# Optimization experiments

Hardware: AMD Instinct MI355X
Metric: run time of the kernel (lower is better)

Reference implementation:

```python
import jax, jax.numpy as jnp
import numpy as np

NUM_L, NUM_W = 10, 10  # num_points_lw


def _local_coords():
    # torch.cartesian_prod(linspace_l, linspace_w) -> (P, 2), l varies slowest
    l = jnp.linspace(-0.5, 0.5, NUM_L)
    w = jnp.linspace(-0.5, 0.5, NUM_W)
    L, W = jnp.meshgrid(l, w, indexing='ij')
    return jnp.stack([L.reshape(-1), W.reshape(-1)], axis=-1)  # (P, 2)


def setup_inputs() -> dict:
    key = jax.random.key(0)
    k1, k2, k3 = jax.random.split(key, 3)
    B, N, T, H, W = 32, 8, 52, 224, 224
    # trajectory states (x, y, vel, yaw, acc, yawvel); positions ~ tens of meters
    x = jax.random.normal(k1, (B, N, T, 6), dtype=jnp.float32) * 5.0
    drivable_map = (jax.random.uniform(k2, (B, H, W)) < 0.7).astype(jnp.float32)
    # realistic vehicle extents (length, width, height)
    extent = jnp.tile(jnp.array([4.5, 2.0, 1.7], jnp.float32), (B, 1)) \
             + 0.2 * jax.random.uniform(k3, (B, 3), dtype=jnp.float32)
    # 2 px/m raster transform centered in the map
    rfa = jnp.array([[2.0, 0.0, W / 2.0], [0.0, 2.0, H / 2.0], [0.0, 0.0, 1.0]],
                    dtype=jnp.float32)
    raster_from_agent = jnp.broadcast_to(rfa, (B, 3, 3))
    return {'x': x, 'drivable_map': drivable_map, 'extent': extent,
            'raster_from_agent': raster_from_agent}


def _forward(x, drivable_map, extent, raster_from_agent):
    B, N, T, _ = x.shape
    _, H, W = drivable_map.shape
    lc = _local_coords()                      # (P, 2)
    P = lc.shape[0]
    M = B * N * T

    traj = x.reshape(M, 6)
    pos = traj[:, :2]                          # (M, 2)
    yaw = traj[:, 3:4]                         # (M, 1)
    lw = jnp.broadcast_to(extent[:, None, None, :], (B, N, T, 3)).reshape(M, 3)[:, :2]
    diag_len = jnp.sqrt(jnp.sum(lw * lw, axis=-1))  # (M,)
    rfa = jnp.broadcast_to(raster_from_agent[:, None, None], (B, N, T, 3, 3)).reshape(M, 3, 3)

    # gen_agt_coords: scale local box grid, rotate, translate
    pts = lc[None, :, :] * lw[:, None, :]      # (M, P, 2)
    s = jnp.sin(yaw)[..., None]                # (M, 1, 1)
    c = jnp.cos(yaw)[..., None]
    rotM = jnp.concatenate([jnp.concatenate([c, s], axis=-1),
                            jnp.concatenate([-s, c], axis=-1)], axis=-2)  # (M, 2, 2)
    agt_pts = pts @ rotM + pos[:, None, :]     # (M, P, 2) agent frame
    # transform_points_tensor: p_pix = R @ p + t (homogeneous 3x3)
    pix = jnp.einsum('mpj,mij->mpi', agt_pts, rfa[:, :2, :2]) + rfa[:, None, :2, 2]
    pix = pix.reshape(B, N, T, P, 2).astype(jnp.int32)   # .long() truncation
    px = jnp.clip(pix[..., 0], 0, W - 1)
    py = jnp.clip(pix[..., 1], 0, H - 1)

    # batch_detect_off_road: gather map values at pixel coords, off-road = 1 - drivable
    drv = jax.vmap(lambda m, ix, iy: m[iy, ix])(drivable_map, px, py)  # (B, N, T, P)
    offroad = 1.0 - drv
    coll = jnp.isclose(offroad, jnp.float32(1.0)).reshape(M, P)  # (M, P) bool

    per_step = jnp.sum(coll, axis=-1)
    overlap = ~((per_step == 0) | (per_step == P))               # (M,) bool

    # pairwise distances (torch.cdist); 2nd copy detached
    a = agt_pts
    b = jax.lax.stop_gradient(agt_pts)
    d2 = (jnp.sum(a * a, -1)[:, :, None] + jnp.sum(b * b, -1)[:, None, :]
          - 2.0 * jnp.einsum('mpd,mqd->mpq', a, b))
    d2 = jnp.maximum(d2, 0.0)
    pos_mask = d2 > 0.0
    dist = jnp.where(pos_mask, jnp.sqrt(jnp.where(pos_mask, d2, 1.0)), 0.0)

    # rows of off-road points -> inf so min is over on-road points
    dist = jnp.where(coll[:, :, None], jnp.inf, dist)
    min_d = jnp.min(dist, axis=1)                                 # (M, P)
    loss_all = 1.0 - min_d / diag_len[:, None]
    loss_off = jnp.where(coll, loss_all, 0.0)
    row_loss = jnp.sum(loss_off, axis=-1)                          # (M,)
    row_loss = jnp.where(overlap, row_loss, 0.0)
    return row_loss.reshape(B, N, T).sum(-1)                       # (B, N)


def reference(x, drivable_map, extent, raster_from_agent):
    return _forward(x, drivable_map, extent, raster_from_agent)
```

## Files before the change

kernel.cpp:

```cpp
#include <hip/hip_runtime.h>
#include <math.h>

#define BB 32
#define NN 8
#define TT 52
#define HH 224
#define WW 224
#define PP 100
#define NWAVE 16

__device__ __forceinline__ float rlane_f(float v, int l) {
    return __int_as_float(__builtin_amdgcn_readlane(__float_as_int(v), l));
}

__global__ __launch_bounds__(NWAVE * 64) void mapcoll_fused(
    const float* __restrict__ x,
    const float* __restrict__ dmap,
    const float* __restrict__ extent,
    const float* __restrict__ rfa,
    float* __restrict__ out)
{
    const int bn   = blockIdx.x;
    const int b    = bn >> 3;
    const int lane = threadIdx.x & 63;
    const int wvu  = __builtin_amdgcn_readfirstlane((int)(threadIdx.x >> 6));

    __shared__ float s_w[NWAVE][128];
    __shared__ float s_part[NWAVE];

    const float lwx = extent[b * 3 + 0];
    const float lwy = extent[b * 3 + 1];
    const float inv_diag = 1.0f / sqrtf(lwx * lwx + lwy * lwy);
    const float r00 = rfa[b*9+0], r01 = rfa[b*9+1], r02 = rfa[b*9+2];
    const float r10 = rfa[b*9+3], r11 = rfa[b*9+4], r12 = rfa[b*9+5];
    const float* __restrict__ map_b = dmap + (size_t)b * (HH * WW);
    const float sx  = lwx * (1.0f / 9.0f);
    const float sy  = lwy * (1.0f / 9.0f);
    const float sy2 = sy * sy;

    float u00 = 0.f, u01 = 0.f, u0c = 0.f, u10 = 0.f, u11 = 0.f, u1c = 0.f;
    if (lane < TT) {
        const int base = (bn * TT + lane) * 6;
        const float2 p2 = *reinterpret_cast<const float2*>(x + base);
        const float yw = x[base + 3];
        const float sn = __sinf(yw), cs = __cosf(yw);
        u00 = cs * r00 + sn * r01;
        u01 = cs * r01 - sn * r00;
        u0c = p2.x * r00 + p2.y * r01 + r02;
        u10 = cs * r10 + sn * r11;
        u11 = cs * r11 - sn * r10;
        u1c = p2.x * r10 + p2.y * r11 + r12;
    }

    const int iA = lane / 10, jA = lane - iA * 10;
    const int pB = lane + 64;
    const int iB = pB / 10,   jB = pB - iB * 10;
    const bool hasB = (lane < PP - 64);
    const float p0A = (-0.5f + (float)iA * (1.0f/9.0f)) * lwx;
    const float p1A = (-0.5f + (float)jA * (1.0f/9.0f)) * lwy;
    const float p0B = (-0.5f + (float)iB * (1.0f/9.0f)) * lwx;
    const float p1B = (-0.5f + (float)jB * (1.0f/9.0f)) * lwy;

    const int shA  = (10 * iA) & 63;
    const int sGA  = (10 * iA - 60) < 0 ? 0 : (10 * iA - 60);
    const int sGB  = ((10 * iB - 60) & 63);
    const int rshA = 31 - jA;
    const int rshB = 31 - jB;

    float di2A[10], di2B[10];
    #pragma unroll
    for (int r = 0; r < 10; ++r) {
        const float dA = (float)(iA - r) * sx; di2A[r] = dA * dA;
        const float dB = (float)(iB - r) * sx; di2B[r] = dB * dB;
    }

    float* wtab = &s_w[wvu][0];
    const unsigned MARK = 1u << 25;

    const int kn = (wvu < 4) ? 4 : 3;
    const int t0 = (wvu < 4) ? (wvu * 4) : (16 + (wvu - 4) * 3);

    float acc = 0.0f;
    #pragma unroll
    for (int k = 0; k < 4; ++k) {
        if (k < kn) {
            const int t = t0 + k;
            const float a00 = rlane_f(u00, t), a01 = rlane_f(u01, t), a0c = rlane_f(u0c, t);
            const float a10 = rlane_f(u10, t), a11 = rlane_f(u11, t), a1c = rlane_f(u1c, t);

            float vAv, vBv = 1.0f;
            {
                const float fx = fmaf(p0A, a00, fmaf(p1A, a01, a0c));
                const float fy = fmaf(p0A, a10, fmaf(p1A, a11, a1c));
                int ix = (int)fx, iy = (int)fy;
                ix = ix < 0 ? 0 : (ix > WW - 1 ? WW - 1 : ix);
                iy = iy < 0 ? 0 : (iy > HH - 1 ? HH - 1 : iy);
                vAv = map_b[iy * WW + ix];
            }
            if (hasB) {
                const float fx = fmaf(p0B, a00, fmaf(p1B, a01, a0c));
                const float fy = fmaf(p0B, a10, fmaf(p1B, a11, a1c));
                int ix = (int)fx, iy = (int)fy;
                ix = ix < 0 ? 0 : (ix > WW - 1 ? WW - 1 : ix);
                iy = iy < 0 ? 0 : (iy > HH - 1 ? HH - 1 : iy);
                vBv = map_b[iy * WW + ix];
            }

            const int clA = (vAv == 0.0f) ? 1 : 0;
            const int clB = (vBv == 0.0f) ? 1 : 0;
            const unsigned long long cmA = __ballot(clA);
            const unsigned long long cmB = __ballot(clB);
            const int ncoll = __popcll(cmA) + __popcll(cmB);
            if (ncoll != 0 && ncoll != PP) {
                const unsigned long long fA = ~cmA;
                const unsigned long long fB = (~cmB) & ((1ull << 36) - 1ull);
                const unsigned long long G  = (fA >> 60) | (fB << 4);

                {
                    const unsigned loA = (unsigned)(fA >> shA);
                    const unsigned gA  = (unsigned)(G  >> sGA);
                    const unsigned m10 = ((iA < 6) ? loA : gA) & 0x3FFu;
                    const unsigned tt  = (m10 >> jA) | (__brev(m10) >> rshA) | MARK;
                    const float d  = (float)__builtin_ctz(tt);
                    const float ds = d * sy;
                    wtab[lane] = ds * ds;
                }
                if (hasB) {
                    const unsigned m10 = ((unsigned)(G >> sGB)) & 0x3FFu;
                    const unsigned tt  = (m10 >> jB) | (__brev(m10) >> rshB) | MARK;
                    const float d  = (float)__builtin_ctz(tt);
                    const float ds = d * sy;
                    wtab[lane + 64] = ds * ds;
                }
                asm volatile("s_waitcnt lgkmcnt(0)" ::: "memory");
                __builtin_amdgcn_wave_barrier();

                float mA = 1e30f, mB = 1e30f;
                #pragma unroll
                for (int r = 0; r < 10; r += 2) {
                    const float wA0 = wtab[r * 10 + jA];
                    const float wA1 = wtab[r * 10 + 10 + jA];
                    mA = fminf(mA, fminf(di2A[r] + wA0, di2A[r + 1] + wA1));
                    const float wB0 = wtab[r * 10 + jB];
                    const float wB1 = wtab[r * 10 + 10 + jB];
                    mB = fminf(mB, fminf(di2B[r] + wB0, di2B[r + 1] + wB1));
                }
                acc += clA ? (1.0f - sqrtf(mA) * inv_diag) : 0.0f;
                acc += clB ? (1.0f - sqrtf(mB) * inv_diag) : 0.0f;
            }
        }
    }

    #pragma unroll
    for (int off = 32; off > 0; off >>= 1) acc += __shfl_down(acc, off);
    if (lane == 0) s_part[wvu] = acc;
    __syncthreads();
    if (threadIdx.x < 64) {
        float v = (lane < NWAVE) ? s_part[lane] : 0.0f;
        v += __shfl_down(v, 8);
        v += __shfl_down(v, 4);
        v += __shfl_down(v, 2);
        v += __shfl_down(v, 1);
        if (lane == 0) out[bn] = v;
    }
}

extern "C" void kernel_launch(void* const* d_in, const int* in_sizes, int n_in,
                              void* d_out, int out_size, void* d_ws, size_t ws_size,
                              hipStream_t stream) {
    const float* x      = (const float*)d_in[0];
    const float* dmap   = (const float*)d_in[1];
    const float* extent = (const float*)d_in[2];
    const float* rfa    = (const float*)d_in[3];
    float* out = (float*)d_out;

    mapcoll_fused<<<BB * NN, NWAVE * 64, 0, stream>>>(x, dmap, extent, rfa, out);
}
```

Baseline: 11.07 us.

## Batch all map gathers before processing timesteps to overlap memory latency

Moves the scattered drivable-map loads for all (up to 4) timesteps per wave to the front so they are in flight together, instead of issuing one timestep's loads and waiting on them before the next. The LDS distance table gets a per-timestep slot, so all tables are written first, followed by a single wave barrier and then the min-distance reductions. This hides global-memory latency and cuts per-step waits, at the cost of more registers and four times the shared memory.

```diff
diff --git a/kernel.cpp b/kernel.cpp
--- a/kernel.cpp
+++ b/kernel.cpp
@@ -25,7 +25,7 @@
     const int lane = threadIdx.x & 63;
     const int wvu  = __builtin_amdgcn_readfirstlane((int)(threadIdx.x >> 6));
 
-    __shared__ float s_w[NWAVE][128];
+    __shared__ float s_w[NWAVE][4][128];
     __shared__ float s_part[NWAVE];
 
     const float lwx = extent[b * 3 + 0];
@@ -36,7 +36,6 @@
     const float* __restrict__ map_b = dmap + (size_t)b * (HH * WW);
     const float sx  = lwx * (1.0f / 9.0f);
     const float sy  = lwy * (1.0f / 9.0f);
-    const float sy2 = sy * sy;
 
     float u00 = 0.f, u01 = 0.f, u0c = 0.f, u10 = 0.f, u11 = 0.f, u1c = 0.f;
     if (lane < TT) {
@@ -74,28 +73,27 @@
         const float dB = (float)(iB - r) * sx; di2B[r] = dB * dB;
     }
 
-    float* wtab = &s_w[wvu][0];
     const unsigned MARK = 1u << 25;
 
     const int kn = (wvu < 4) ? 4 : 3;
     const int t0 = (wvu < 4) ? (wvu * 4) : (16 + (wvu - 4) * 3);
 
-    float acc = 0.0f;
+    float vA[4], vB[4];
     #pragma unroll
     for (int k = 0; k < 4; ++k) {
+        vA[k] = 1.0f;
+        vB[k] = 1.0f;
         if (k < kn) {
             const int t = t0 + k;
             const float a00 = rlane_f(u00, t), a01 = rlane_f(u01, t), a0c = rlane_f(u0c, t);
             const float a10 = rlane_f(u10, t), a11 = rlane_f(u11, t), a1c = rlane_f(u1c, t);
-
-            float vAv, vBv = 1.0f;
             {
                 const float fx = fmaf(p0A, a00, fmaf(p1A, a01, a0c));
                 const float fy = fmaf(p0A, a10, fmaf(p1A, a11, a1c));
                 int ix = (int)fx, iy = (int)fy;
                 ix = ix < 0 ? 0 : (ix > WW - 1 ? WW - 1 : ix);
                 iy = iy < 0 ? 0 : (iy > HH - 1 ? HH - 1 : iy);
-                vAv = map_b[iy * WW + ix];
+                vA[k] = map_b[iy * WW + ix];
             }
             if (hasB) {
                 const float fx = fmaf(p0B, a00, fmaf(p1B, a01, a0c));
@@ -103,19 +101,25 @@
                 int ix = (int)fx, iy = (int)fy;
                 ix = ix < 0 ? 0 : (ix > WW - 1 ? WW - 1 : ix);
                 iy = iy < 0 ? 0 : (iy > HH - 1 ? HH - 1 : iy);
-                vBv = map_b[iy * WW + ix];
+                vB[k] = map_b[iy * WW + ix];
             }
+        }
+    }
 
-            const int clA = (vAv == 0.0f) ? 1 : 0;
-            const int clB = (vBv == 0.0f) ? 1 : 0;
+    int liveMask = 0;
+    #pragma unroll
+    for (int k = 0; k < 4; ++k) {
+        if (k < kn) {
+            const int clA = (vA[k] == 0.0f) ? 1 : 0;
+            const int clB = (vB[k] == 0.0f) ? 1 : 0;
             const unsigned long long cmA = __ballot(clA);
             const unsigned long long cmB = __ballot(clB);
             const int ncoll = __popcll(cmA) + __popcll(cmB);
             if (ncoll != 0 && ncoll != PP) {
+                liveMask |= (1 << k);
                 const unsigned long long fA = ~cmA;
                 const unsigned long long fB = (~cmB) & ((1ull << 36) - 1ull);
                 const unsigned long long G  = (fA >> 60) | (fB << 4);
-
                 {
                     const unsigned loA = (unsigned)(fA >> shA);
                     const unsigned gA  = (unsigned)(G  >> sGA);
@@ -123,31 +127,38 @@
                     const unsigned tt  = (m10 >> jA) | (__brev(m10) >> rshA) | MARK;
                     const float d  = (float)__builtin_ctz(tt);
                     const float ds = d * sy;
-                    wtab[lane] = ds * ds;
+                    s_w[wvu][k][lane] = ds * ds;
                 }
                 if (hasB) {
                     const unsigned m10 = ((unsigned)(G >> sGB)) & 0x3FFu;
                     const unsigned tt  = (m10 >> jB) | (__brev(m10) >> rshB) | MARK;
                     const float d  = (float)__builtin_ctz(tt);
                     const float ds = d * sy;
-                    wtab[lane + 64] = ds * ds;
+                    s_w[wvu][k][lane + 64] = ds * ds;
                 }
-                asm volatile("s_waitcnt lgkmcnt(0)" ::: "memory");
-                __builtin_amdgcn_wave_barrier();
+            }
+        }
+    }
+    asm volatile("s_waitcnt lgkmcnt(0)" ::: "memory");
+    __builtin_amdgcn_wave_barrier();
 
-                float mA = 1e30f, mB = 1e30f;
-                #pragma unroll
-                for (int r = 0; r < 10; r += 2) {
-                    const float wA0 = wtab[r * 10 + jA];
-                    const float wA1 = wtab[r * 10 + 10 + jA];
-                    mA = fminf(mA, fminf(di2A[r] + wA0, di2A[r + 1] + wA1));
-                    const float wB0 = wtab[r * 10 + jB];
-                    const float wB1 = wtab[r * 10 + 10 + jB];
-                    mB = fminf(mB, fminf(di2B[r] + wB0, di2B[r + 1] + wB1));
-                }
-                acc += clA ? (1.0f - sqrtf(mA) * inv_diag) : 0.0f;
-                acc += clB ? (1.0f - sqrtf(mB) * inv_diag) : 0.0f;
+    float acc = 0.0f;
+    #pragma unroll
+    for (int k = 0; k < 4; ++k) {
+        if ((liveMask >> k) & 1) {
+            const float* wt = &s_w[wvu][k][0];
+            float mA = 1e30f, mB = 1e30f;
+            #pragma unroll
+            for (int r = 0; r < 10; r += 2) {
+                const float wA0 = wt[r * 10 + jA];
+                const float wA1 = wt[r * 10 + 10 + jA];
+                mA = fminf(mA, fminf(di2A[r] + wA0, di2A[r + 1] + wA1));
+                const float wB0 = wt[r * 10 + jB];
+                const float wB1 = wt[r * 10 + 10 + jB];
+                mB = fminf(mB, fminf(di2B[r] + wB0, di2B[r + 1] + wB1));
             }
+            acc += (vA[k] == 0.0f) ? (1.0f - sqrtf(mA) * inv_diag) : 0.0f;
+            acc += (vB[k] == 0.0f) ? (1.0f - sqrtf(mB) * inv_diag) : 0.0f;
         }
     }
 
```

Measured after the change: 11.11 us. Within noise of the previous version (+0.3%).
